# Kernel optimization log

Measured on AMD Instinct MI355X. Metric: run time of the kernel, lower is better.

The kernel has to match this reference:

```python
import jax, jax.numpy as jnp
import numpy as np

B, T, C = 2, 2048, 2048
H, D = 16, 128  # num_heads, head_dim


def setup_inputs() -> dict:
    key = jax.random.key(0)
    ks = jax.random.split(key, 5)
    x = jax.random.normal(ks[0], (B, T, C), dtype=jnp.float32)
    # causal mask: mask==0 positions are filled with -inf
    mask = jnp.tril(jnp.ones((T, T), dtype=jnp.int32))[None, None, :, :]
    wq = jax.random.normal(ks[1], (C, C), dtype=jnp.float32) * (C ** -0.5)
    wk = jax.random.normal(ks[2], (C, C), dtype=jnp.float32) * (C ** -0.5)
    wv = jax.random.normal(ks[3], (C, C), dtype=jnp.float32) * (C ** -0.5)
    wo = jax.random.normal(ks[4], (C, C), dtype=jnp.float32) * (C ** -0.5)
    return {"x": x, "mask": mask, "wq": wq, "wk": wk, "wv": wv, "wo": wo}


def reference(x, mask, wq, wk, wv, wo):
    Bx, Tx, Cx = x.shape
    scale = D ** -0.5
    # torch Linear: y = x @ W.T (weights are [out, in])
    q = (x @ wq.T).reshape(Bx, Tx, H, D).transpose(0, 2, 1, 3)  # [B,H,T,D]
    k = (x @ wk.T).reshape(Bx, Tx, H, D).transpose(0, 2, 1, 3)
    v = (x @ wv.T).reshape(Bx, Tx, H, D).transpose(0, 2, 1, 3)
    scores = jnp.einsum("bhqd,bhkd->bhqk", q, k) * scale  # [B,H,T,T]
    scores = jnp.where(mask == 0, -jnp.inf, scores)
    attn = jax.nn.softmax(scores, axis=-1)
    out = jnp.einsum("bhqk,bhkd->bhqd", attn, v)  # [B,H,T,D]
    out = out.transpose(0, 2, 1, 3).reshape(Bx, Tx, Cx)
    return out @ wo.T
```

## Files before the change

### kernel.cpp

```cpp
#include <hip/hip_runtime.h>
#include <hip/hip_bf16.h>


#define BB 2
#define TT 2048
#define CC 2048
#define HH 16
#define DD 128
#define MM (BB*TT)
#define NQT (TT/64)
#define GNT (CC/64)

typedef __bf16 bf16x8 __attribute__((ext_vector_type(8)));
typedef __bf16 bf16x4 __attribute__((ext_vector_type(4)));
typedef float  f32x4  __attribute__((ext_vector_type(4)));

#define MFMA16(a, b, c) __builtin_amdgcn_mfma_f32_16x16x32_bf16((a), (b), (c), 0, 0, 0)

__device__ __forceinline__ void g2lds16(const void* g, void* l) {
    __builtin_amdgcn_global_load_lds(
        (const __attribute__((address_space(1))) void*)g,
        (__attribute__((address_space(3))) void*)l,
        16, 0, 0);
}

__global__ __launch_bounds__(256) void cvt_all(
    const float* __restrict__ x,  const float* __restrict__ wq,
    const float* __restrict__ wk, const float* __restrict__ wv,
    const float* __restrict__ wo, __bf16* __restrict__ out_base)
{
    const int idx = blockIdx.x * 256 + threadIdx.x;
    const float* in; int off;
    if (idx < (1 << 21)) { in = x; off = idx; }
    else {
        const int r = idx - (1 << 21);
        const int k = r >> 20;
        in  = (k == 0) ? wq : (k == 1) ? wk : (k == 2) ? wv : wo;
        off = r & ((1 << 20) - 1);
    }
    const float4 v = ((const float4*)in)[off];
    bf16x4 o;
    o.x = (__bf16)v.x; o.y = (__bf16)v.y;
    o.z = (__bf16)v.z; o.w = (__bf16)v.w;
    ((bf16x4*)out_base)[idx] = o;
}

template<int MODE>
__global__ __launch_bounds__(512, 2) void gemm_bt(
    const __bf16* __restrict__ A, const __bf16* __restrict__ Wt,
    void* __restrict__ out)
{
    __shared__ __align__(16) __bf16 As[3][256*64];
    __shared__ __align__(16) __bf16 Bs[3][2][128*32];

    const int tid = threadIdx.x;
    const int w   = tid >> 6, lane = tid & 63;
    const int wm  = w >> 1,  wn  = w & 1;
    const int lo  = lane & 15, hi = lane >> 4;
    const int xr  = (lo & 7) << 4;
    const int xb2 = ((lo >> 1) & 3) << 4;

    const int bid   = blockIdx.y * gridDim.x + blockIdx.x;
    const int xcd   = bid & 7, loc = bid >> 3;
    const int n0    = (2*xcd + (loc & 1)) * 128;
    const int m0    = (loc >> 1) * 256;

    const int ar   = tid >> 3, as_ = tid & 7;
    const int acol = ((as_ ^ (ar & 7)) << 3);
    const int br   = tid >> 2, bs_ = tid & 3;
    const int bcol = ((bs_ ^ ((br >> 1) & 3)) << 3);

    auto stageA3a = [&](int buf, int kt) {
        #pragma unroll
        for (int j = 0; j < 3; ++j)
            g2lds16(A + (size_t)(m0 + j*64 + ar)*CC + kt*64 + acol,
                    (char*)&As[buf][0] + j*8192 + w*1024);
    };
    auto stageA3b = [&](int buf, int kt) {
        g2lds16(A + (size_t)(m0 + 3*64 + ar)*CC + kt*64 + acol,
                (char*)&As[buf][0] + 3*8192 + w*1024);
        #pragma unroll
        for (int kh = 0; kh < 2; ++kh)
            g2lds16(Wt + (size_t)(n0 + br)*CC + kt*64 + kh*32 + bcol,
                    (char*)&Bs[buf][kh][0] + w*1024);
    };
    auto rdA = [&](bf16x8* af, int buf, int ks) {
        const char* base = (const char*)&As[buf][0];
        #pragma unroll
        for (int mf = 0; mf < 4; ++mf) {
            const int r = wm*64 + mf*16 + lo;
            af[mf] = *(const bf16x8*)(base + r*128 + ((ks*64 + hi*16) ^ xr));
        }
    };
    auto rdB = [&](bf16x8* bv, int buf, int ks) {
        const char* base = (const char*)&Bs[buf][ks][0];
        #pragma unroll
        for (int nf = 0; nf < 4; ++nf) {
            const int n = wn*64 + nf*16 + lo;
            bv[nf] = *(const bf16x8*)(base + n*64 + ((hi*16) ^ xb2));
        }
    };

    f32x4 acc[4][4] = {};

    stageA3a(0, 0); stageA3b(0, 0);
    stageA3a(1, 1); stageA3b(1, 1);
    asm volatile("s_waitcnt vmcnt(6)" ::: "memory");
    __builtin_amdgcn_s_barrier();

    int rb = 0;
    #pragma unroll 1
    for (int t = 0; t < GNT - 2; ++t) {
        const int sb = (rb == 0) ? 2 : rb - 1;
        {
            bf16x8 af[4], bv[4];
            rdA(af, rb, 0); rdB(bv, rb, 0);
            stageA3a(sb, t + 2);
            __builtin_amdgcn_s_barrier();
            __builtin_amdgcn_s_setprio(1);
            #pragma unroll
            for (int mf = 0; mf < 4; ++mf)
                #pragma unroll
                for (int nf = 0; nf < 4; ++nf)
                    acc[mf][nf] = MFMA16(af[mf], bv[nf], acc[mf][nf]);
            __builtin_amdgcn_s_setprio(0);
            __builtin_amdgcn_s_barrier();
        }
        {
            bf16x8 af[4], bv[4];
            rdA(af, rb, 1); rdB(bv, rb, 1);
            stageA3b(sb, t + 2);
            __builtin_amdgcn_s_barrier();
            __builtin_amdgcn_s_setprio(1);
            #pragma unroll
            for (int mf = 0; mf < 4; ++mf)
                #pragma unroll
                for (int nf = 0; nf < 4; ++nf)
                    acc[mf][nf] = MFMA16(af[mf], bv[nf], acc[mf][nf]);
            __builtin_amdgcn_s_setprio(0);
            asm volatile("s_waitcnt vmcnt(6)" ::: "memory");
            __builtin_amdgcn_s_barrier();
        }
        rb = (rb == 2) ? 0 : rb + 1;
    }
    {
        bf16x8 af[4], bv[4];
        rdA(af, rb, 0); rdB(bv, rb, 0);
        __builtin_amdgcn_s_barrier();
        #pragma unroll
        for (int mf = 0; mf < 4; ++mf)
            #pragma unroll
            for (int nf = 0; nf < 4; ++nf)
                acc[mf][nf] = MFMA16(af[mf], bv[nf], acc[mf][nf]);
        __builtin_amdgcn_s_barrier();
        rdA(af, rb, 1); rdB(bv, rb, 1);
        #pragma unroll
        for (int mf = 0; mf < 4; ++mf)
            #pragma unroll
            for (int nf = 0; nf < 4; ++nf)
                acc[mf][nf] = MFMA16(af[mf], bv[nf], acc[mf][nf]);
        asm volatile("s_waitcnt vmcnt(0)" ::: "memory");
        __builtin_amdgcn_s_barrier();
        rb = (rb == 2) ? 0 : rb + 1;
    }
    {
        bf16x8 af[4], bv[4];
        rdA(af, rb, 0); rdB(bv, rb, 0);
        #pragma unroll
        for (int mf = 0; mf < 4; ++mf)
            #pragma unroll
            for (int nf = 0; nf < 4; ++nf)
                acc[mf][nf] = MFMA16(af[mf], bv[nf], acc[mf][nf]);
        rdA(af, rb, 1); rdB(bv, rb, 1);
        #pragma unroll
        for (int mf = 0; mf < 4; ++mf)
            #pragma unroll
            for (int nf = 0; nf < 4; ++nf)
                acc[mf][nf] = MFMA16(af[mf], bv[nf], acc[mf][nf]);
    }

    #pragma unroll
    for (int mf = 0; mf < 4; ++mf) {
        #pragma unroll
        for (int nf = 0; nf < 4; ++nf) {
            #pragma unroll
            for (int r = 0; r < 4; ++r) {
                const int row = m0 + wm*64 + mf*16 + hi*4 + r;
                const int col = n0 + wn*64 + nf*16 + lo;
                const float v = acc[mf][nf][r];
                if (MODE == 0) {
                    const int b = row >> 11, t = row & (TT-1);
                    const int h = col >> 7,  d = col & (DD-1);
                    ((__bf16*)out)[(size_t)((b*HH + h)*TT + t)*DD + d] = (__bf16)v;
                } else if (MODE == 1) {
                    const int b = row >> 11, t = row & (TT-1);
                    const int h = col >> 7,  d = col & (DD-1);
                    ((__bf16*)out)[(size_t)((b*HH + h)*DD + d)*TT + t] = (__bf16)v;
                } else {
                    ((float*)out)[(size_t)row*CC + col] = v;
                }
            }
        }
    }
}

__global__ __launch_bounds__(256, 2) void attn_fwd(
    const __bf16* __restrict__ Q, const __bf16* __restrict__ K,
    const __bf16* __restrict__ Vt, __bf16* __restrict__ O)
{
    __shared__ __align__(16) __bf16 Ks[2][64*128];
    __shared__ __align__(16) __bf16 Vs[2][128*64];
    __shared__ __align__(16) __bf16 Ps[4][16*64];

    const int lid   = blockIdx.y * gridDim.x + blockIdx.x;
    const int bh    = lid & 31;
    const int pairx = lid >> 5;
    const int tid = threadIdx.x;
    const int w   = tid >> 6, lane = tid & 63;
    const int lo  = lane & 15, hi = lane >> 4;
    const int xr  = (lo & 7) << 4;

    const int krow_l  = lane >> 4;
    const int kcol_sw = ((lane & 15) << 4);
    const int vrow_l  = lane >> 3;
    const int vcol_sw = (((lane & 7) ^ (lane >> 3)) << 3);

    const size_t kbase = (size_t)bh * TT * DD;
    const size_t vbase = (size_t)bh * DD * TT;
    const int b = bh >> 4, h = bh & 15;
    const float SC = 0.12754613142f;

    bf16x8 vones;
    #pragma unroll
    for (int i = 0; i < 8; ++i) vones[i] = (__bf16)1.0f;

    auto stage = [&](int buf, int kv0) {
        #pragma unroll
        for (int i = 0; i < 4; ++i) {
            const int c = 4*w + i;
            {
                const int row = 4*c + krow_l;
                const int sw  = (kcol_sw ^ ((row & 7) << 4)) >> 1;
                g2lds16(K + kbase + (size_t)(kv0 + row)*DD + sw,
                        &Ks[buf][0] + c*512);
            }
            {
                const int row = 8*c + vrow_l;
                g2lds16(Vt + vbase + (size_t)row*TT + kv0 + vcol_sw,
                        &Vs[buf][0] + c*512);
            }
        }
    };

    #pragma unroll 1
    for (int half = 0; half < 2; ++half) {
        const int qt = half ? pairx : (NQT - 1 - pairx);
        const int q0 = qt * 64;

        const __bf16* Qbase = Q + (kbase + (size_t)(q0 + w*16 + lo) * DD);
        bf16x8 qf[4];
        #pragma unroll
        for (int kc = 0; kc < 4; ++kc)
            qf[kc] = *(const bf16x8*)(Qbase + kc*32 + hi*8);

        float mrow[4];
        #pragma unroll
        for (int r = 0; r < 4; ++r) mrow[r] = -1e30f;
        f32x4 oacc[8] = {};
        f32x4 sacc = {};

        const int qg_base = q0 + w*16 + hi*4;
        const int ntiles  = qt + 1;

        stage(0, 0);
        __syncthreads();
        int cur = 0;

        for (int t = 0; t < ntiles; ++t) {
            const int kv0 = t*64;
            if (t + 1 < ntiles) stage(cur ^ 1, (t+1)*64);

            const char* Kb = (const char*)&Ks[cur][0];
            const char* Vb = (const char*)&Vs[cur][0];

            f32x4 s[4];
            __builtin_amdgcn_s_setprio(1);
            #pragma unroll
            for (int st = 0; st < 4; ++st) {
                f32x4 a = {};
                #pragma unroll
                for (int kc = 0; kc < 4; ++kc) {
                    const bf16x8 kf = *(const bf16x8*)(
                        Kb + (st*16 + lo)*256 + ((kc*64 + hi*16) ^ xr));
                    a = MFMA16(qf[kc], kf, a);
                }
                s[st] = a;
            }
            __builtin_amdgcn_s_setprio(0);

            float pmax[4];
            const bool diag = (t == ntiles - 1);
            #pragma unroll
            for (int r = 0; r < 4; ++r) {
                const int qg = qg_base + r;
                float mx = -1e30f;
                #pragma unroll
                for (int st = 0; st < 4; ++st) {
                    float v = s[st][r] * SC;
                    if (diag) {
                        const int kvg = kv0 + st*16 + lo;
                        v = (kvg > qg) ? -1e30f : v;
                    }
                    s[st][r] = v;
                    mx = fmaxf(mx, v);
                }
                #pragma unroll
                for (int msk = 1; msk < 16; msk <<= 1)
                    mx = fmaxf(mx, __shfl_xor(mx, msk, 64));
                pmax[r] = mx;
            }

            bool need = false;
            #pragma unroll
            for (int r = 0; r < 4; ++r)
                need = need || (pmax[r] > mrow[r] + 11.5f);
            if (__any(need)) {
                float rsc[4];
                #pragma unroll
                for (int r = 0; r < 4; ++r) {
                    const float mnew = fmaxf(mrow[r], pmax[r]);
                    rsc[r]  = __builtin_amdgcn_exp2f(mrow[r] - mnew);
                    mrow[r] = mnew;
                    sacc[r] *= rsc[r];
                }
                #pragma unroll
                for (int dc = 0; dc < 8; ++dc)
                    #pragma unroll
                    for (int r = 0; r < 4; ++r)
                        oacc[dc][r] *= rsc[r];
            }

            #pragma unroll
            for (int r = 0; r < 4; ++r)
                #pragma unroll
                for (int st = 0; st < 4; ++st)
                    s[st][r] = __builtin_amdgcn_exp2f(s[st][r] - mrow[r]);

            char* Pw = (char*)&Ps[w][0];
            #pragma unroll
            for (int st = 0; st < 4; ++st)
                #pragma unroll
                for (int r = 0; r < 4; ++r) {
                    const int row = hi*4 + r;
                    *(__bf16*)(Pw + row*128 + (((st*16 + lo)*2) ^ ((row & 7) << 4)))
                        = (__bf16)s[st][r];
                }

            __builtin_amdgcn_s_setprio(1);
            #pragma unroll
            for (int kc2 = 0; kc2 < 2; ++kc2) {
                const bf16x8 pf = *(const bf16x8*)(
                    Pw + lo*128 + ((kc2*64 + hi*16) ^ xr));
                #pragma unroll
                for (int dc = 0; dc < 8; ++dc) {
                    const bf16x8 vf = *(const bf16x8*)(
                        Vb + (dc*16 + lo)*128 + ((kc2*64 + hi*16) ^ xr));
                    oacc[dc] = MFMA16(pf, vf, oacc[dc]);
                }
                sacc = MFMA16(pf, vones, sacc);
            }
            __builtin_amdgcn_s_setprio(0);

            __syncthreads();
            cur ^= 1;
        }

        #pragma unroll
        for (int r = 0; r < 4; ++r) {
            const float inv = 1.f / sacc[r];
            const int qg = qg_base + r;
            #pragma unroll
            for (int dc = 0; dc < 8; ++dc) {
                const int d = dc*16 + lo;
                O[(size_t)(b*TT + qg)*CC + h*DD + d] = (__bf16)(oacc[dc][r] * inv);
            }
        }
    }
}

extern "C" void kernel_launch(void* const* d_in, const int* in_sizes, int n_in,
                              void* d_out, int out_size, void* d_ws, size_t ws_size,
                              hipStream_t stream) {
    const float* x  = (const float*)d_in[0];
    const float* wq = (const float*)d_in[2];
    const float* wk = (const float*)d_in[3];
    const float* wv = (const float*)d_in[4];
    const float* wo = (const float*)d_in[5];

    char* p = (char*)d_ws;
    __bf16* xb  = (__bf16*)p; p += (size_t)MM*CC*2;
    __bf16* wqb = (__bf16*)p; p += (size_t)CC*CC*2;
    __bf16* wkb = (__bf16*)p; p += (size_t)CC*CC*2;
    __bf16* wvb = (__bf16*)p; p += (size_t)CC*CC*2;
    __bf16* wob = (__bf16*)p; p += (size_t)CC*CC*2;
    __bf16* Qb  = (__bf16*)p; p += (size_t)MM*CC*2;
    __bf16* Kb  = (__bf16*)p; p += (size_t)MM*CC*2;
    __bf16* Vtb = (__bf16*)p; p += (size_t)MM*CC*2;
    __bf16* AOb = xb;

    cvt_all<<<24576, 256, 0, stream>>>(x, wq, wk, wv, wo, xb);

    const dim3 gg(CC/128, MM/256);
    gemm_bt<0><<<gg, 512, 0, stream>>>(xb, wqb, Qb);
    gemm_bt<0><<<gg, 512, 0, stream>>>(xb, wkb, Kb);
    gemm_bt<1><<<gg, 512, 0, stream>>>(xb, wvb, Vtb);

    attn_fwd<<<dim3(NQT/2, BB*HH), 256, 0, stream>>>(Qb, Kb, Vtb, AOb);

    gemm_bt<2><<<gg, 512, 0, stream>>>(AOb, wob, (void*)d_out);
}
```

Before: 239.9 us.

## Enlarge attention query tile to 128 rows with two sub-tiles per wave

Each attention block now handles a single 128-row query tile, with every wave owning 32 rows as two 16-row sub-tiles, instead of processing two 64-row tiles one after the other. Each K/V fragment loaded from LDS feeds two MFMAs, which halves K/V staging traffic per query row. Load balancing changes from pairing tiles inside a block to ordering blocks by descending tile work. In exchange, register pressure doubles for accumulators and Q fragments, and the P buffer in LDS grows.

```diff
diff --git a/kernel.cpp b/kernel.cpp
--- a/kernel.cpp
+++ b/kernel.cpp
@@ -8,7 +8,7 @@
 #define HH 16
 #define DD 128
 #define MM (BB*TT)
-#define NQT (TT/64)
+#define NQB (TT/128)
 #define GNT (CC/64)
 
 typedef __bf16 bf16x8 __attribute__((ext_vector_type(8)));
@@ -210,11 +210,13 @@
 {
     __shared__ __align__(16) __bf16 Ks[2][64*128];
     __shared__ __align__(16) __bf16 Vs[2][128*64];
-    __shared__ __align__(16) __bf16 Ps[4][16*64];
-
-    const int lid   = blockIdx.y * gridDim.x + blockIdx.x;
-    const int bh    = lid & 31;
-    const int pairx = lid >> 5;
+    __shared__ __align__(16) __bf16 Ps[4][32*64];
+
+    const int bh = blockIdx.x;
+    const int qy = blockIdx.y;
+    const int qt = (qy < 8) ? (15 - qy) : (qy - 8);
+    const int q0 = qt * 128;
+
     const int tid = threadIdx.x;
     const int w   = tid >> 6, lane = tid & 63;
     const int lo  = lane & 15, hi = lane >> 4;
@@ -252,137 +254,156 @@
         }
     };
 
-    #pragma unroll 1
-    for (int half = 0; half < 2; ++half) {
-        const int qt = half ? pairx : (NQT - 1 - pairx);
-        const int q0 = qt * 64;
-
-        const __bf16* Qbase = Q + (kbase + (size_t)(q0 + w*16 + lo) * DD);
-        bf16x8 qf[4];
+    const __bf16* Qbase = Q + (kbase + (size_t)(q0 + w*32 + lo) * DD);
+    bf16x8 qf[2][4];
+    #pragma unroll
+    for (int i = 0; i < 2; ++i)
         #pragma unroll
         for (int kc = 0; kc < 4; ++kc)
-            qf[kc] = *(const bf16x8*)(Qbase + kc*32 + hi*8);
-
-        float mrow[4];
-        #pragma unroll
-        for (int r = 0; r < 4; ++r) mrow[r] = -1e30f;
-        f32x4 oacc[8] = {};
-        f32x4 sacc = {};
-
-        const int qg_base = q0 + w*16 + hi*4;
-        const int ntiles  = qt + 1;
-
-        stage(0, 0);
-        __syncthreads();
-        int cur = 0;
-
-        for (int t = 0; t < ntiles; ++t) {
-            const int kv0 = t*64;
-            if (t + 1 < ntiles) stage(cur ^ 1, (t+1)*64);
-
-            const char* Kb = (const char*)&Ks[cur][0];
-            const char* Vb = (const char*)&Vs[cur][0];
-
-            f32x4 s[4];
-            __builtin_amdgcn_s_setprio(1);
-            #pragma unroll
-            for (int st = 0; st < 4; ++st) {
-                f32x4 a = {};
-                #pragma unroll
-                for (int kc = 0; kc < 4; ++kc) {
-                    const bf16x8 kf = *(const bf16x8*)(
-                        Kb + (st*16 + lo)*256 + ((kc*64 + hi*16) ^ xr));
-                    a = MFMA16(qf[kc], kf, a);
-                }
-                s[st] = a;
-            }
-            __builtin_amdgcn_s_setprio(0);
-
-            float pmax[4];
-            const bool diag = (t == ntiles - 1);
+            qf[i][kc] = *(const bf16x8*)(Qbase + (size_t)i*16*DD + kc*32 + hi*8);
+
+    float mrow[2][4];
+    #pragma unroll
+    for (int i = 0; i < 2; ++i)
+        #pragma unroll
+        for (int r = 0; r < 4; ++r) mrow[i][r] = -1e30f;
+    f32x4 oacc[2][8] = {};
+    f32x4 sacc[2] = {};
+
+    const int qgb = q0 + w*32 + hi*4;
+    const int ntiles = 2*(qt + 1);
+
+    stage(0, 0);
+    __syncthreads();
+    int cur = 0;
+
+    for (int t = 0; t < ntiles; ++t) {
+        const int kv0 = t*64;
+        if (t + 1 < ntiles) stage(cur ^ 1, (t+1)*64);
+
+        const char* Kb = (const char*)&Ks[cur][0];
+        const char* Vb = (const char*)&Vs[cur][0];
+
+        f32x4 s[2][4];
+        __builtin_amdgcn_s_setprio(1);
+        #pragma unroll
+        for (int st = 0; st < 4; ++st) {
+            f32x4 a0 = {}, a1 = {};
+            #pragma unroll
+            for (int kc = 0; kc < 4; ++kc) {
+                const bf16x8 kf = *(const bf16x8*)(
+                    Kb + (st*16 + lo)*256 + ((kc*64 + hi*16) ^ xr));
+                a0 = MFMA16(qf[0][kc], kf, a0);
+                a1 = MFMA16(qf[1][kc], kf, a1);
+            }
+            s[0][st] = a0; s[1][st] = a1;
+        }
+        __builtin_amdgcn_s_setprio(0);
+
+        float pmax[2][4];
+        const bool diag = (t >= ntiles - 2);
+        #pragma unroll
+        for (int i = 0; i < 2; ++i) {
             #pragma unroll
             for (int r = 0; r < 4; ++r) {
-                const int qg = qg_base + r;
+                const int qg = qgb + i*16 + r;
                 float mx = -1e30f;
                 #pragma unroll
                 for (int st = 0; st < 4; ++st) {
-                    float v = s[st][r] * SC;
+                    float v = s[i][st][r] * SC;
                     if (diag) {
                         const int kvg = kv0 + st*16 + lo;
                         v = (kvg > qg) ? -1e30f : v;
                     }
-                    s[st][r] = v;
+                    s[i][st][r] = v;
                     mx = fmaxf(mx, v);
                 }
                 #pragma unroll
                 for (int msk = 1; msk < 16; msk <<= 1)
                     mx = fmaxf(mx, __shfl_xor(mx, msk, 64));
-                pmax[r] = mx;
-            }
-
-            bool need = false;
+                pmax[i][r] = mx;
+            }
+        }
+
+        bool need = false;
+        #pragma unroll
+        for (int i = 0; i < 2; ++i)
             #pragma unroll
             for (int r = 0; r < 4; ++r)
-                need = need || (pmax[r] > mrow[r] + 11.5f);
-            if (__any(need)) {
-                float rsc[4];
+                need = need || (pmax[i][r] > mrow[i][r] + 11.5f);
+        if (__any(need)) {
+            float rsc[2][4];
+            #pragma unroll
+            for (int i = 0; i < 2; ++i)
                 #pragma unroll
                 for (int r = 0; r < 4; ++r) {
-                    const float mnew = fmaxf(mrow[r], pmax[r]);
-                    rsc[r]  = __builtin_amdgcn_exp2f(mrow[r] - mnew);
-                    mrow[r] = mnew;
-                    sacc[r] *= rsc[r];
+                    const float mnew = fmaxf(mrow[i][r], pmax[i][r]);
+                    rsc[i][r] = __builtin_amdgcn_exp2f(mrow[i][r] - mnew);
+                    mrow[i][r] = mnew;
+                    sacc[i][r] *= rsc[i][r];
                 }
+            #pragma unroll
+            for (int i = 0; i < 2; ++i)
                 #pragma unroll
                 for (int dc = 0; dc < 8; ++dc)
                     #pragma unroll
                     for (int r = 0; r < 4; ++r)
-                        oacc[dc][r] *= rsc[r];
-            }
-
+                        oacc[i][dc][r] *= rsc[i][r];
+        }
+
+        #pragma unroll
+        for (int i = 0; i < 2; ++i)
             #pragma unroll
             for (int r = 0; r < 4; ++r)
                 #pragma unroll
                 for (int st = 0; st < 4; ++st)
-                    s[st][r] = __builtin_amdgcn_exp2f(s[st][r] - mrow[r]);
-
-            char* Pw = (char*)&Ps[w][0];
+                    s[i][st][r] = __builtin_amdgcn_exp2f(s[i][st][r] - mrow[i][r]);
+
+        char* Pw = (char*)&Ps[w][0];
+        #pragma unroll
+        for (int i = 0; i < 2; ++i)
             #pragma unroll
             for (int st = 0; st < 4; ++st)
                 #pragma unroll
                 for (int r = 0; r < 4; ++r) {
-                    const int row = hi*4 + r;
+                    const int row = i*16 + hi*4 + r;
                     *(__bf16*)(Pw + row*128 + (((st*16 + lo)*2) ^ ((row & 7) << 4)))
-                        = (__bf16)s[st][r];
+                        = (__bf16)s[i][st][r];
                 }
 
-            __builtin_amdgcn_s_setprio(1);
-            #pragma unroll
-            for (int kc2 = 0; kc2 < 2; ++kc2) {
-                const bf16x8 pf = *(const bf16x8*)(
-                    Pw + lo*128 + ((kc2*64 + hi*16) ^ xr));
-                #pragma unroll
-                for (int dc = 0; dc < 8; ++dc) {
-                    const bf16x8 vf = *(const bf16x8*)(
-                        Vb + (dc*16 + lo)*128 + ((kc2*64 + hi*16) ^ xr));
-                    oacc[dc] = MFMA16(pf, vf, oacc[dc]);
-                }
-                sacc = MFMA16(pf, vones, sacc);
-            }
-            __builtin_amdgcn_s_setprio(0);
-
-            __syncthreads();
-            cur ^= 1;
-        }
-
+        __builtin_amdgcn_s_setprio(1);
+        #pragma unroll
+        for (int kc2 = 0; kc2 < 2; ++kc2) {
+            const bf16x8 pf0 = *(const bf16x8*)(
+                Pw + lo*128 + ((kc2*64 + hi*16) ^ xr));
+            const bf16x8 pf1 = *(const bf16x8*)(
+                Pw + (16 + lo)*128 + ((kc2*64 + hi*16) ^ xr));
+            #pragma unroll
+            for (int dc = 0; dc < 8; ++dc) {
+                const bf16x8 vf = *(const bf16x8*)(
+                    Vb + (dc*16 + lo)*128 + ((kc2*64 + hi*16) ^ xr));
+                oacc[0][dc] = MFMA16(pf0, vf, oacc[0][dc]);
+                oacc[1][dc] = MFMA16(pf1, vf, oacc[1][dc]);
+            }
+            sacc[0] = MFMA16(pf0, vones, sacc[0]);
+            sacc[1] = MFMA16(pf1, vones, sacc[1]);
+        }
+        __builtin_amdgcn_s_setprio(0);
+
+        __syncthreads();
+        cur ^= 1;
+    }
+
+    #pragma unroll
+    for (int i = 0; i < 2; ++i) {
         #pragma unroll
         for (int r = 0; r < 4; ++r) {
-            const float inv = 1.f / sacc[r];
-            const int qg = qg_base + r;
+            const float inv = 1.f / sacc[i][r];
+            const int qg = qgb + i*16 + r;
             #pragma unroll
             for (int dc = 0; dc < 8; ++dc) {
                 const int d = dc*16 + lo;
-                O[(size_t)(b*TT + qg)*CC + h*DD + d] = (__bf16)(oacc[dc][r] * inv);
+                O[(size_t)(b*TT + qg)*CC + h*DD + d] = (__bf16)(oacc[i][dc][r] * inv);
             }
         }
     }
@@ -415,7 +436,7 @@
     gemm_bt<0><<<gg, 512, 0, stream>>>(xb, wkb, Kb);
     gemm_bt<1><<<gg, 512, 0, stream>>>(xb, wvb, Vtb);
 
-    attn_fwd<<<dim3(NQT/2, BB*HH), 256, 0, stream>>>(Qb, Kb, Vtb, AOb);
+    attn_fwd<<<dim3(BB*HH, NQB), 256, 0, stream>>>(Qb, Kb, Vtb, AOb);
 
     gemm_bt<2><<<gg, 512, 0, stream>>>(AOb, wob, (void*)d_out);
 }
```

New measurement: 261.0 us. 1.09x slower.
